# Kernel tuning notes

Measured on AMD Instinct MI355X. Metric: run time of the kernel, lower is better.

## Reference

```python
import jax, jax.numpy as jnp
import numpy as np

N = 50000        # nodes
E = 600000       # edges (before self loops)
F_IN = 128       # num_features
HID = 64         # hidden_channels
NC = 10          # num_classes
NG = 64          # graphs in batch
NEG_SLOPE = 0.2  # PyG GATv2 default


def setup_inputs() -> dict:
    key = jax.random.key(0)
    ks = jax.random.split(key, 13)
    s = lambda d: np.float32(1.0 / np.sqrt(d))
    x = jax.random.normal(ks[0], (N, F_IN), jnp.float32)
    edge_index = jax.random.randint(ks[1], (2, E), 0, N, dtype=jnp.int64)
    batch = jnp.sort(jax.random.randint(ks[2], (N,), 0, NG, dtype=jnp.int64))
    # conv1: heads=2, concat=True -> out dim 2*HID
    Wl1 = jax.random.normal(ks[3], (F_IN, 2 * HID), jnp.float32) * s(F_IN)
    Wr1 = jax.random.normal(ks[4], (F_IN, 2 * HID), jnp.float32) * s(F_IN)
    att1 = jax.random.normal(ks[5], (2, HID), jnp.float32) * s(HID)
    b1 = jnp.zeros((2 * HID,), jnp.float32)
    # conv2: heads=1, concat=False -> out dim HID
    Wl2 = jax.random.normal(ks[6], (2 * HID, HID), jnp.float32) * s(2 * HID)
    Wr2 = jax.random.normal(ks[7], (2 * HID, HID), jnp.float32) * s(2 * HID)
    att2 = jax.random.normal(ks[8], (1, HID), jnp.float32) * s(HID)
    b2 = jnp.zeros((HID,), jnp.float32)
    Wlin = jax.random.normal(ks[9], (HID, NC), jnp.float32) * s(HID)
    blin = jnp.zeros((NC,), jnp.float32)
    return {"x": x, "edge_index": edge_index, "batch": batch,
            "Wl1": Wl1, "Wr1": Wr1, "att1": att1, "b1": b1,
            "Wl2": Wl2, "Wr2": Wr2, "att2": att2, "b2": b2,
            "Wlin": Wlin, "blin": blin}


def _gatv2(x, Wl, Wr, att, b, src, dst, heads, ch, concat):
    """PyG GATv2Conv: e = a^T LeakyReLU(W_l x_j + W_r x_i), softmax over dst."""
    n = x.shape[0]
    xl = (x @ Wl).reshape(n, heads, ch)   # source-side transform
    xr = (x @ Wr).reshape(n, heads, ch)   # destination-side transform
    m = jax.nn.leaky_relu(xl[src] + xr[dst], NEG_SLOPE)  # [E, H, C]
    e = jnp.einsum('ehc,hc->eh', m, att)                 # [E, H]
    emax = jax.ops.segment_max(e, dst, num_segments=n)   # stable softmax per dst
    p = jnp.exp(e - emax[dst])
    denom = jax.ops.segment_sum(p, dst, num_segments=n)
    alpha = p / denom[dst]                               # [E, H]
    out = jax.ops.segment_sum(alpha[:, :, None] * xl[src], dst, num_segments=n)
    out = out.reshape(n, heads * ch) if concat else out.mean(axis=1)
    return out + b


def reference(x, edge_index, batch, Wl1, Wr1, att1, b1, Wl2, Wr2, att2, b2, Wlin, blin):
    loops = jnp.arange(N, dtype=edge_index.dtype)        # add_self_loops=True
    src = jnp.concatenate([edge_index[0], loops])
    dst = jnp.concatenate([edge_index[1], loops])
    h = jax.nn.elu(_gatv2(x, Wl1, Wr1, att1, b1, src, dst, 2, HID, True))
    h = jax.nn.elu(_gatv2(h, Wl2, Wr2, att2, b2, src, dst, 1, HID, False))
    # global_mean_pool
    pooled = jax.ops.segment_sum(h, batch, num_segments=NG)
    counts = jnp.maximum(
        jax.ops.segment_sum(jnp.ones((N,), h.dtype), batch, num_segments=NG), 1.0)
    g = pooled / counts[:, None]
    # dropout(p=0.4) is identity in eval mode
    return g @ Wlin + blin
```

## Files before the change

kernel.cpp:

```cpp
#include <hip/hip_runtime.h>
#include <hip/hip_fp16.h>
#include <cstdint>
#include <cstddef>


typedef __attribute__((ext_vector_type(8))) short s8v;
typedef __attribute__((ext_vector_type(4))) float f4v;

#define LOG2E 1.44269504f

__device__ __forceinline__ unsigned short f2bf(float f) {
    unsigned u = __float_as_uint(f);
    unsigned r = (u + 0x7fffu + ((u >> 16) & 1u)) >> 16;
    return (unsigned short)r;
}
__device__ __forceinline__ __half2 habs2_(__half2 x) {
    unsigned u; __builtin_memcpy(&u, &x, 4);
    u &= 0x7fff7fffu;
    __half2 r; __builtin_memcpy(&r, &u, 4);
    return r;
}
__device__ __forceinline__ float elu_(float v) {
    return v > 0.f ? v : exp2f(v * LOG2E) - 1.f;
}
union U4H { uint4 u; __half2 h[4]; };

template<int CO, bool ELU_A>
__device__ __forceinline__ void gemm_dual_body(
        int blk, const void* __restrict__ Aptr,
        const unsigned short* __restrict__ Wlp, const unsigned short* __restrict__ Wrp,
        __half* __restrict__ outL, __half* __restrict__ outR,
        const float* __restrict__ att, const float* __restrict__ bias_in,
        float* __restrict__ sl06, float* __restrict__ sr06, int n) {
    constexpr int NT = CO / 16;
    constexpr int H  = CO / 64;
    int lane = threadIdx.x & 63;
    int node0 = blk * 64 + (threadIdx.x >> 6) * 16;
    int m = lane & 15, quad = lane >> 4;
    int row = node0 + m;
    s8v a[4];
#pragma unroll
    for (int ks = 0; ks < 4; ks++) {
        union { s8v v; unsigned short u[8]; } t;
        int k0 = ks * 32 + quad * 8;
        if (row < n) {
            if (ELU_A) {
                const unsigned short* A = (const unsigned short*)Aptr;
                uint4 raw = *(const uint4*)(A + ((unsigned)row << 7) + k0);
                float4 bA = *(const float4*)(bias_in + k0);
                float4 bB = *(const float4*)(bias_in + k0 + 4);
                float bb[8] = {bA.x, bA.y, bA.z, bA.w, bB.x, bB.y, bB.z, bB.w};
                unsigned rr[4] = {raw.x, raw.y, raw.z, raw.w};
#pragma unroll
                for (int jp = 0; jp < 4; jp++) {
                    float e0 = elu_(__uint_as_float(rr[jp] << 16)         + bb[jp * 2]);
                    float e1 = elu_(__uint_as_float(rr[jp] & 0xffff0000u) + bb[jp * 2 + 1]);
                    t.u[jp * 2]     = f2bf(e0);
                    t.u[jp * 2 + 1] = f2bf(e1);
                }
            } else {
                const float* A = (const float*)Aptr;
                float4 fA = *(const float4*)(A + ((unsigned)row << 7) + k0);
                float4 fB = *(const float4*)(A + ((unsigned)row << 7) + k0 + 4);
                t.u[0] = f2bf(fA.x); t.u[1] = f2bf(fA.y);
                t.u[2] = f2bf(fA.z); t.u[3] = f2bf(fA.w);
                t.u[4] = f2bf(fB.x); t.u[5] = f2bf(fB.y);
                t.u[6] = f2bf(fB.z); t.u[7] = f2bf(fB.w);
            }
        } else {
#pragma unroll
            for (int j = 0; j < 8; j++) t.u[j] = 0;
        }
        a[ks] = t.v;
    }
    float dl[2] = {0.f, 0.f}, dr[2] = {0.f, 0.f};
#pragma unroll
    for (int ct = 0; ct < NT; ct++) {
        f4v cl = {0.f, 0.f, 0.f, 0.f}, cr = {0.f, 0.f, 0.f, 0.f};
#pragma unroll
        for (int ks = 0; ks < 4; ks++) {
            s8v bl = *(const s8v*)(Wlp + ((size_t)(ct * 4 + ks) * 64 + lane) * 8);
            s8v br = *(const s8v*)(Wrp + ((size_t)(ct * 4 + ks) * 64 + lane) * 8);
            cl = __builtin_amdgcn_mfma_f32_16x16x32_bf16(bl, a[ks], cl, 0, 0, 0);
            cr = __builtin_amdgcn_mfma_f32_16x16x32_bf16(br, a[ks], cr, 0, 0, 0);
        }
        int ch0 = ct * 16 + quad * 4;
        int hh = (H == 2) ? (ct >> 2) : 0;
        float4 av = *(const float4*)(att + ch0);
        dl[hh] += av.x * cl[0] + av.y * cl[1] + av.z * cl[2] + av.w * cl[3];
        dr[hh] += av.x * cr[0] + av.y * cr[1] + av.z * cr[2] + av.w * cr[3];
        if (row < n) {
            __half2 p0 = __floats2half2_rn(cl[0], cl[1]);
            __half2 p1 = __floats2half2_rn(cl[2], cl[3]);
            __half2 q0 = __floats2half2_rn(cr[0], cr[1]);
            __half2 q1 = __floats2half2_rn(cr[2], cr[3]);
            uint2 ov, orv;
            __builtin_memcpy(&ov.x, &p0, 4);  __builtin_memcpy(&ov.y, &p1, 4);
            __builtin_memcpy(&orv.x, &q0, 4); __builtin_memcpy(&orv.y, &q1, 4);
            *(uint2*)(outL + (unsigned)row * CO + ch0) = ov;
            *(uint2*)(outR + (unsigned)row * CO + ch0) = orv;
        }
    }
#pragma unroll
    for (int h = 0; h < H; h++) {
        float vl = dl[h], vr = dr[h];
        vl += __shfl_xor(vl, 16, 64); vl += __shfl_xor(vl, 32, 64);
        vr += __shfl_xor(vr, 16, 64); vr += __shfl_xor(vr, 32, 64);
        if (quad == 0 && row < n) {
            if (H == 2) {
                sl06[((unsigned)row << 1) + h] = (0.6f * LOG2E) * vl;
                sr06[((unsigned)row << 1) + h] = (0.6f * LOG2E) * vr;
            } else {
                sl06[row] = (0.6f * LOG2E) * vl;
                sr06[row] = (0.6f * LOG2E) * vr;
            }
        }
    }
}

__global__ void pack_zero(const float* __restrict__ Wl1, const float* __restrict__ Wr1,
                          const float* __restrict__ Wl2, const float* __restrict__ Wr2,
                          unsigned short* __restrict__ Wl1p, unsigned short* __restrict__ Wr1p,
                          unsigned short* __restrict__ Wl2p, unsigned short* __restrict__ Wr2p,
                          int* __restrict__ cnt, int n, int zcb,
                          float* __restrict__ pooled, int npool) {
    int b = blockIdx.x;
    if (b >= 24) {
        if (b < 24 + zcb) {
            int i = (b - 24) * 256 + threadIdx.x;
            if (i < n) cnt[i] = 0;
        } else {
            int i = (b - 24 - zcb) * 256 + threadIdx.x;
            if (i < npool) pooled[i] = 0.f;
        }
        return;
    }
    int t = b * 256 + threadIdx.x;
    const float* W; unsigned short* Wp; int CO, base;
    if      (t < 2048) { W = Wl1; Wp = Wl1p; CO = 128; base = t; }
    else if (t < 4096) { W = Wr1; Wp = Wr1p; CO = 128; base = t - 2048; }
    else if (t < 5120) { W = Wl2; Wp = Wl2p; CO = 64;  base = t - 4096; }
    else               { W = Wr2; Wp = Wr2p; CO = 64;  base = t - 5120; }
    int lane = base & 63, ks = (base >> 6) & 3, ct = base >> 8;
    int col = ct * 16 + (lane & 15);
    int k0 = ks * 32 + (lane >> 4) * 8;
    unsigned short u[8];
#pragma unroll
    for (int j = 0; j < 8; j++) u[j] = f2bf(W[(size_t)(k0 + j) * CO + col]);
    unsigned* dst = (unsigned*)(Wp + (size_t)base * 8);
    dst[0] = u[0] | ((unsigned)u[1] << 16);
    dst[1] = u[2] | ((unsigned)u[3] << 16);
    dst[2] = u[4] | ((unsigned)u[5] << 16);
    dst[3] = u[6] | ((unsigned)u[7] << 16);
}

__global__ void gemm1_fill(const float* __restrict__ x,
                           const unsigned short* __restrict__ Wl1p,
                           const unsigned short* __restrict__ Wr1p,
                           __half* __restrict__ xl1, __half* __restrict__ xr1,
                           const float* __restrict__ att1,
                           float* __restrict__ sl1, float* __restrict__ sr1, int n, int GB,
                           const int* __restrict__ srcA, const int* __restrict__ dstA, int E,
                           int* __restrict__ cnt, int* __restrict__ bucket) {
    if ((int)blockIdx.x < GB) {
        gemm_dual_body<128, false>(blockIdx.x, x, Wl1p, Wr1p, xl1, xr1,
                                   att1, nullptr, sl1, sr1, n);
        return;
    }
    int i = (blockIdx.x - GB) * 256 + threadIdx.x;
    if (i < E) {
        int d = dstA[i];
        int pos = atomicAdd(&cnt[d], 1);
        bucket[(d << 6) + pos] = srcA[i];
    }
}

__global__ void gemm2(const unsigned short* __restrict__ h1,
                      const unsigned short* __restrict__ Wl2p,
                      const unsigned short* __restrict__ Wr2p,
                      __half* __restrict__ xl2, __half* __restrict__ xr2,
                      const float* __restrict__ att2, const float* __restrict__ b1,
                      float* __restrict__ sl2, float* __restrict__ sr2, int n) {
    gemm_dual_body<64, true>(blockIdx.x, h1, Wl2p, Wr2p, xl2, xr2,
                             att2, b1, sl2, sr2, n);
}

__global__ void gat1_fused(const __half* __restrict__ xl, const __half* __restrict__ xr,
                           const float* __restrict__ sl06, const float* __restrict__ sr06,
                           const float* __restrict__ att,
                           const int* __restrict__ cnt, const int* __restrict__ bucket,
                           unsigned short* __restrict__ h1, int n) {
    int d = (blockIdx.x * blockDim.x + threadIdx.x) >> 6;
    if (d >= n) return;
    int lane = threadIdx.x & 63;
    int e = lane >> 4;
    int h = (lane >> 3) & 1;
    int off = h * 64 + (lane & 7) * 8;
    U4H xv; xv.u = *(const uint4*)(xr + (((unsigned)d << 7) + off));
    float4 aA = *(const float4*)(att + off);
    float4 aB = *(const float4*)(att + off + 4);
    const float S = 0.4f * LOG2E;
    __half2 a2[4];
    a2[0] = __floats2half2_rn(S * aA.x, S * aA.y);
    a2[1] = __floats2half2_rn(S * aA.z, S * aA.w);
    a2[2] = __floats2half2_rn(S * aB.x, S * aB.y);
    a2[3] = __floats2half2_rn(S * aB.z, S * aB.w);
    float srd = sr06[((unsigned)d << 1) + h];
    float c0 = 0.f, c1 = 0.f, c2 = 0.f, c3 = 0.f;
    float c4 = 0.f, c5 = 0.f, c6 = 0.f, c7 = 0.f, den = 0.f;
    int deg = cnt[d];
    int bb = d << 6;
    int j0 = -1 + e;
    int sA = bucket[bb + max(j0, 0)];  sA = (j0 >= 0 && j0 < deg) ? sA : d;
    int j1 = j0 + 4;
    int sB = bucket[bb + min(max(j1, 0), 63)];  sB = (j1 >= 0 && j1 < deg) ? sB : d;
    U4H xc; xc.u = *(const uint4*)(xl + (((unsigned)sA << 7) + off));
    float slc = sl06[((unsigned)sA << 1) + h];
    for (int base = -1; base < deg; base += 4) {
        U4H xn; xn.u = *(const uint4*)(xl + (((unsigned)sB << 7) + off));
        float sln = sl06[((unsigned)sB << 1) + h];
        int jC = base + 8 + e;
        int sC = bucket[bb + min(max(jC, 0), 63)];
        sC = (jC >= 0 && jC < deg) ? sC : d;
        bool valid = (base + e) < deg;
        __half2 sc = __floats2half2_rn(0.f, 0.f);
        sc = __hfma2(a2[0], habs2_(__hadd2(xc.h[0], xv.h[0])), sc);
        sc = __hfma2(a2[1], habs2_(__hadd2(xc.h[1], xv.h[1])), sc);
        sc = __hfma2(a2[2], habs2_(__hadd2(xc.h[2], xv.h[2])), sc);
        sc = __hfma2(a2[3], habs2_(__hadd2(xc.h[3], xv.h[3])), sc);
        float v = __low2float(sc) + __high2float(sc);
        v += __shfl_xor(v, 1, 64); v += __shfl_xor(v, 2, 64); v += __shfl_xor(v, 4, 64);
        float p = valid ? exp2f(slc + srd + v) : 0.f;
        c0 = fmaf(__low2float(xc.h[0]),  p, c0);
        c1 = fmaf(__high2float(xc.h[0]), p, c1);
        c2 = fmaf(__low2float(xc.h[1]),  p, c2);
        c3 = fmaf(__high2float(xc.h[1]), p, c3);
        c4 = fmaf(__low2float(xc.h[2]),  p, c4);
        c5 = fmaf(__high2float(xc.h[2]), p, c5);
        c6 = fmaf(__low2float(xc.h[3]),  p, c6);
        c7 = fmaf(__high2float(xc.h[3]), p, c7);
        den += p;
        xc = xn; slc = sln; sB = sC;
    }
#pragma unroll
    for (int o = 16; o <= 32; o <<= 1) {
        c0 += __shfl_xor(c0, o, 64); c1 += __shfl_xor(c1, o, 64);
        c2 += __shfl_xor(c2, o, 64); c3 += __shfl_xor(c3, o, 64);
        c4 += __shfl_xor(c4, o, 64); c5 += __shfl_xor(c5, o, 64);
        c6 += __shfl_xor(c6, o, 64); c7 += __shfl_xor(c7, o, 64);
        den += __shfl_xor(den, o, 64);
    }
    if (e == 0) {
        float r = 1.f / den;
        uint4 out;
        out.x = (unsigned)f2bf(c0 * r) | ((unsigned)f2bf(c1 * r) << 16);
        out.y = (unsigned)f2bf(c2 * r) | ((unsigned)f2bf(c3 * r) << 16);
        out.z = (unsigned)f2bf(c4 * r) | ((unsigned)f2bf(c5 * r) << 16);
        out.w = (unsigned)f2bf(c6 * r) | ((unsigned)f2bf(c7 * r) << 16);
        *(uint4*)(h1 + (((unsigned)d << 7) + off)) = out;
    }
}

__global__ void gat2_fused(const __half* __restrict__ xl, const __half* __restrict__ xr,
                           const float* __restrict__ sl06, const float* __restrict__ sr06,
                           const float* __restrict__ att,
                           const int* __restrict__ cnt, const int* __restrict__ bucket,
                           float* __restrict__ h2, int n) {
    int d = (blockIdx.x * blockDim.x + threadIdx.x) >> 6;
    if (d >= n) return;
    int lane = threadIdx.x & 63;
    int e = lane >> 3;
    int off = (lane & 7) * 8;
    U4H xv; xv.u = *(const uint4*)(xr + (((unsigned)d << 6) + off));
    float4 aA = *(const float4*)(att + off);
    float4 aB = *(const float4*)(att + off + 4);
    const float S = 0.4f * LOG2E;
    __half2 a2[4];
    a2[0] = __floats2half2_rn(S * aA.x, S * aA.y);
    a2[1] = __floats2half2_rn(S * aA.z, S * aA.w);
    a2[2] = __floats2half2_rn(S * aB.x, S * aB.y);
    a2[3] = __floats2half2_rn(S * aB.z, S * aB.w);
    float srd = sr06[d];
    float c0 = 0.f, c1 = 0.f, c2 = 0.f, c3 = 0.f;
    float c4 = 0.f, c5 = 0.f, c6 = 0.f, c7 = 0.f, den = 0.f;
    int deg = cnt[d];
    int bb = d << 6;
    int j0 = -1 + e;
    int sA = bucket[bb + max(j0, 0)];  sA = (j0 >= 0 && j0 < deg) ? sA : d;
    int j1 = j0 + 8;
    int sB = bucket[bb + min(max(j1, 0), 63)];  sB = (j1 >= 0 && j1 < deg) ? sB : d;
    U4H xc; xc.u = *(const uint4*)(xl + (((unsigned)sA << 6) + off));
    float slc = sl06[sA];
    for (int base = -1; base < deg; base += 8) {
        U4H xn; xn.u = *(const uint4*)(xl + (((unsigned)sB << 6) + off));
        float sln = sl06[sB];
        int jC = base + 16 + e;
        int sC = bucket[bb + min(max(jC, 0), 63)];
        sC = (jC >= 0 && jC < deg) ? sC : d;
        bool valid = (base + e) < deg;
        __half2 sc = __floats2half2_rn(0.f, 0.f);
        sc = __hfma2(a2[0], habs2_(__hadd2(xc.h[0], xv.h[0])), sc);
        sc = __hfma2(a2[1], habs2_(__hadd2(xc.h[1], xv.h[1])), sc);
        sc = __hfma2(a2[2], habs2_(__hadd2(xc.h[2], xv.h[2])), sc);
        sc = __hfma2(a2[3], habs2_(__hadd2(xc.h[3], xv.h[3])), sc);
        float v = __low2float(sc) + __high2float(sc);
        v += __shfl_xor(v, 1, 64); v += __shfl_xor(v, 2, 64); v += __shfl_xor(v, 4, 64);
        float p = valid ? exp2f(slc + srd + v) : 0.f;
        c0 = fmaf(__low2float(xc.h[0]),  p, c0);
        c1 = fmaf(__high2float(xc.h[0]), p, c1);
        c2 = fmaf(__low2float(xc.h[1]),  p, c2);
        c3 = fmaf(__high2float(xc.h[1]), p, c3);
        c4 = fmaf(__low2float(xc.h[2]),  p, c4);
        c5 = fmaf(__high2float(xc.h[2]), p, c5);
        c6 = fmaf(__low2float(xc.h[3]),  p, c6);
        c7 = fmaf(__high2float(xc.h[3]), p, c7);
        den += p;
        xc = xn; slc = sln; sB = sC;
    }
#pragma unroll
    for (int o = 8; o <= 32; o <<= 1) {
        c0 += __shfl_xor(c0, o, 64); c1 += __shfl_xor(c1, o, 64);
        c2 += __shfl_xor(c2, o, 64); c3 += __shfl_xor(c3, o, 64);
        c4 += __shfl_xor(c4, o, 64); c5 += __shfl_xor(c5, o, 64);
        c6 += __shfl_xor(c6, o, 64); c7 += __shfl_xor(c7, o, 64);
        den += __shfl_xor(den, o, 64);
    }
    if (e == 0) {
        float r = 1.f / den;
        float4 A = {c0 * r, c1 * r, c2 * r, c3 * r};
        float4 B = {c4 * r, c5 * r, c6 * r, c7 * r};
        *(float4*)(h2 + (((unsigned)d << 6) + off))     = A;
        *(float4*)(h2 + (((unsigned)d << 6) + off + 4)) = B;
    }
}

__global__ void pool_rle(const float* __restrict__ h, const float* __restrict__ b2,
                         const int* __restrict__ batch,
                         int n, int chunk, float* __restrict__ pooled,
                         float* __restrict__ counts) {
    int w = (blockIdx.x * blockDim.x + threadIdx.x) >> 6;
    int lane = threadIdx.x & 63;
    int start = w * chunk;
    int end = min(n, start + chunk);
    if (start >= end) return;
    float bv = b2[lane];
    int cur = batch[start];
    float acc = 0.f, cnt = 0.f;
    for (int node = start; node < end; node++) {
        int g = batch[node];
        if (g != cur) {
            atomicAdd(&pooled[(size_t)cur * 64 + lane], acc);
            if (lane == 0) atomicAdd(&counts[cur], cnt);
            acc = 0.f; cnt = 0.f; cur = g;
        }
        acc += elu_(h[((unsigned)node << 6) + lane] + bv);
        cnt += 1.f;
    }
    atomicAdd(&pooled[(size_t)cur * 64 + lane], acc);
    if (lane == 0) atomicAdd(&counts[cur], cnt);
}

__global__ void head(const float* __restrict__ pooled, const float* __restrict__ counts,
                     const float* __restrict__ Wlin, const float* __restrict__ blin,
                     float* __restrict__ out, int NC) {
    int g = blockIdx.x;
    int lane = threadIdx.x;
    float cnt = fmaxf(counts[g], 1.f);
    float v = pooled[(size_t)g * 64 + lane] / cnt;
    for (int j = 0; j < NC; j++) {
        float t = v * Wlin[lane * NC + j];
        for (int off = 32; off > 0; off >>= 1) t += __shfl_down(t, off, 64);
        if (lane == 0) out[g * NC + j] = t + blin[j];
    }
}

extern "C" void kernel_launch(void* const* d_in, const int* in_sizes, int n_in,
                              void* d_out, int out_size, void* d_ws, size_t ws_size,
                              hipStream_t stream) {
    const float* x    = (const float*)d_in[0];
    const int*   ei   = (const int*)d_in[1];
    const int*   batch= (const int*)d_in[2];
    const float* Wl1  = (const float*)d_in[3];
    const float* Wr1  = (const float*)d_in[4];
    const float* att1 = (const float*)d_in[5];
    const float* b1   = (const float*)d_in[6];
    const float* Wl2  = (const float*)d_in[7];
    const float* Wr2  = (const float*)d_in[8];
    const float* att2 = (const float*)d_in[9];
    const float* b2   = (const float*)d_in[10];
    const float* Wlin = (const float*)d_in[11];
    const float* blin = (const float*)d_in[12];

    const int n    = in_sizes[0] / 128;
    const int E    = in_sizes[1] / 2;
    const int NC   = in_sizes[12];
    const int NG   = out_size / NC;

    const int* srcA = ei;
    const int* dstA = ei + E;

    uint8_t* w = (uint8_t*)d_ws;
    const size_t rowB = (size_t)n * 128 * 2;
    __half*         xl1 = (__half*)w;
    __half*         xr1 = (__half*)(w + rowB);
    unsigned short* h1  = (unsigned short*)(w + 2 * rowB);
    __half*         xl2 = (__half*)w;
    __half*         xr2 = (__half*)(w + (size_t)n * 64 * 2);
    float*          h2  = (float*)(w + rowB);
    uint8_t* fx = w + 3 * rowB;
    unsigned short* Wl1p = (unsigned short*)fx;            fx += 16384 * 2;
    unsigned short* Wr1p = (unsigned short*)fx;            fx += 16384 * 2;
    unsigned short* Wl2p = (unsigned short*)fx;            fx += 8192 * 2;
    unsigned short* Wr2p = (unsigned short*)fx;            fx += 8192 * 2;
    float* sl1 = (float*)fx;                               fx += (size_t)n * 2 * 4;
    float* sr1 = (float*)fx;                               fx += (size_t)n * 2 * 4;
    float* sl2 = (float*)fx;                               fx += (size_t)n * 4;
    float* sr2 = (float*)fx;                               fx += (size_t)n * 4;
    float* pooled = (float*)fx;                            fx += (size_t)NG * 64 * 4;
    float* counts = (float*)fx;                            fx += (size_t)NG * 4;
    int* cnt    = (int*)fx;                                fx += (size_t)n * 4;
    int* bucket = (int*)fx;                                fx += ((size_t)n * 64 + 64) * 4;
    if (ws_size < (size_t)(fx - (uint8_t*)d_ws)) return;

    const int GB  = (n + 63) / 64;
    const int zcb = (n + 255) / 256;
    const int npool = NG * 65;
    const int pzb = (npool + 255) / 256;
    const int FB  = (E + 255) / 256;
    const int dblocks = (n + 3) / 4;

    pack_zero<<<24 + zcb + pzb, 256, 0, stream>>>(Wl1, Wr1, Wl2, Wr2,
                                                  Wl1p, Wr1p, Wl2p, Wr2p,
                                                  cnt, n, zcb, pooled, npool);
    gemm1_fill<<<GB + FB, 256, 0, stream>>>(x, Wl1p, Wr1p, xl1, xr1, att1,
                                            sl1, sr1, n, GB,
                                            srcA, dstA, E, cnt, bucket);
    gat1_fused<<<dblocks, 256, 0, stream>>>(xl1, xr1, sl1, sr1, att1,
                                            cnt, bucket, h1, n);
    gemm2<<<GB, 256, 0, stream>>>(h1, Wl2p, Wr2p, xl2, xr2, att2, b1, sl2, sr2, n);
    gat2_fused<<<dblocks, 256, 0, stream>>>(xl2, xr2, sl2, sr2, att2,
                                            cnt, bucket, h2, n);
    {
        const int nwaves = 1024;
        const int chunk = (n + nwaves - 1) / nwaves;
        pool_rle<<<256, 256, 0, stream>>>(h2, b2, batch, n, chunk, pooled, counts);
    }
    head<<<NG, 64, 0, stream>>>(pooled, counts, Wlin, blin, (float*)d_out, NC);
}
```

Before: 233.9 us.

## Interleave GEMM and edge-fill blocks, deepen gather prefetch, store h1 as fp16

The gemm1_fill launch now alternates GEMM blocks and edge-bucketing blocks by blockIdx parity, and each fill thread handles four edges, so the two kinds of work run side by side instead of GEMM blocks going first. Both GAT aggregation kernels now prefetch neighbour rows two iterations ahead instead of one, which should hide more gather latency at the cost of extra registers. The h1 intermediate is stored as fp16 instead of bf16, which makes packing cheaper and keeps more mantissa bits but has a smaller dynamic range.

```diff
diff --git a/kernel.cpp b/kernel.cpp
--- a/kernel.cpp
+++ b/kernel.cpp
@@ -45,16 +45,15 @@
         int k0 = ks * 32 + quad * 8;
         if (row < n) {
             if (ELU_A) {
-                const unsigned short* A = (const unsigned short*)Aptr;
-                uint4 raw = *(const uint4*)(A + ((unsigned)row << 7) + k0);
+                const __half* A = (const __half*)Aptr;
+                U4H raw; raw.u = *(const uint4*)(A + ((unsigned)row << 7) + k0);
                 float4 bA = *(const float4*)(bias_in + k0);
                 float4 bB = *(const float4*)(bias_in + k0 + 4);
                 float bb[8] = {bA.x, bA.y, bA.z, bA.w, bB.x, bB.y, bB.z, bB.w};
-                unsigned rr[4] = {raw.x, raw.y, raw.z, raw.w};
 #pragma unroll
                 for (int jp = 0; jp < 4; jp++) {
-                    float e0 = elu_(__uint_as_float(rr[jp] << 16)         + bb[jp * 2]);
-                    float e1 = elu_(__uint_as_float(rr[jp] & 0xffff0000u) + bb[jp * 2 + 1]);
+                    float e0 = elu_(__low2float(raw.h[jp])  + bb[jp * 2]);
+                    float e1 = elu_(__high2float(raw.h[jp]) + bb[jp * 2 + 1]);
                     t.u[jp * 2]     = f2bf(e0);
                     t.u[jp * 2 + 1] = f2bf(e1);
                 }
@@ -159,23 +158,34 @@
                            const unsigned short* __restrict__ Wr1p,
                            __half* __restrict__ xl1, __half* __restrict__ xr1,
                            const float* __restrict__ att1,
-                           float* __restrict__ sl1, float* __restrict__ sr1, int n, int GB,
+                           float* __restrict__ sl1, float* __restrict__ sr1, int n,
+                           int GB, int FBn,
                            const int* __restrict__ srcA, const int* __restrict__ dstA, int E,
                            int* __restrict__ cnt, int* __restrict__ bucket) {
-    if ((int)blockIdx.x < GB) {
-        gemm_dual_body<128, false>(blockIdx.x, x, Wl1p, Wr1p, xl1, xr1,
-                                   att1, nullptr, sl1, sr1, n);
+    int b = blockIdx.x;
+    if ((b & 1) == 0) {
+        int g = b >> 1;
+        if (g < GB)
+            gemm_dual_body<128, false>(g, x, Wl1p, Wr1p, xl1, xr1,
+                                       att1, nullptr, sl1, sr1, n);
         return;
     }
-    int i = (blockIdx.x - GB) * 256 + threadIdx.x;
-    if (i < E) {
-        int d = dstA[i];
-        int pos = atomicAdd(&cnt[d], 1);
-        bucket[(d << 6) + pos] = srcA[i];
-    }
-}
-
-__global__ void gemm2(const unsigned short* __restrict__ h1,
+    int f = b >> 1;
+    if (f >= FBn) return;
+    int t0 = f * 256 + threadIdx.x;
+    int Q = FBn * 256;
+#pragma unroll
+    for (int k = 0; k < 4; k++) {
+        int i = t0 + k * Q;
+        if (i < E) {
+            int d = dstA[i];
+            int pos = atomicAdd(&cnt[d], 1);
+            bucket[(d << 6) + pos] = srcA[i];
+        }
+    }
+}
+
+__global__ void gemm2(const __half* __restrict__ h1,
                       const unsigned short* __restrict__ Wl2p,
                       const unsigned short* __restrict__ Wr2p,
                       __half* __restrict__ xl2, __half* __restrict__ xr2,
@@ -189,7 +199,7 @@
                            const float* __restrict__ sl06, const float* __restrict__ sr06,
                            const float* __restrict__ att,
                            const int* __restrict__ cnt, const int* __restrict__ bucket,
-                           unsigned short* __restrict__ h1, int n) {
+                           __half* __restrict__ h1, int n) {
     int d = (blockIdx.x * blockDim.x + threadIdx.x) >> 6;
     if (d >= n) return;
     int lane = threadIdx.x & 63;
@@ -211,17 +221,21 @@
     int deg = cnt[d];
     int bb = d << 6;
     int j0 = -1 + e;
-    int sA = bucket[bb + max(j0, 0)];  sA = (j0 >= 0 && j0 < deg) ? sA : d;
+    int s0 = bucket[bb + max(j0, 0)];          s0 = (j0 >= 0 && j0 < deg) ? s0 : d;
     int j1 = j0 + 4;
-    int sB = bucket[bb + min(max(j1, 0), 63)];  sB = (j1 >= 0 && j1 < deg) ? sB : d;
-    U4H xc; xc.u = *(const uint4*)(xl + (((unsigned)sA << 7) + off));
-    float slc = sl06[((unsigned)sA << 1) + h];
+    int s1 = bucket[bb + min(max(j1, 0), 63)]; s1 = (j1 >= 0 && j1 < deg) ? s1 : d;
+    int j2 = j0 + 8;
+    int s2 = bucket[bb + min(max(j2, 0), 63)]; s2 = (j2 >= 0 && j2 < deg) ? s2 : d;
+    U4H xc;  xc.u  = *(const uint4*)(xl + (((unsigned)s0 << 7) + off));
+    float slc = sl06[((unsigned)s0 << 1) + h];
+    U4H xn1; xn1.u = *(const uint4*)(xl + (((unsigned)s1 << 7) + off));
+    float sln1 = sl06[((unsigned)s1 << 1) + h];
     for (int base = -1; base < deg; base += 4) {
-        U4H xn; xn.u = *(const uint4*)(xl + (((unsigned)sB << 7) + off));
-        float sln = sl06[((unsigned)sB << 1) + h];
-        int jC = base + 8 + e;
-        int sC = bucket[bb + min(max(jC, 0), 63)];
-        sC = (jC >= 0 && jC < deg) ? sC : d;
+        U4H xn2; xn2.u = *(const uint4*)(xl + (((unsigned)s2 << 7) + off));
+        float sln2 = sl06[((unsigned)s2 << 1) + h];
+        int j3 = base + 12 + e;
+        int s3 = bucket[bb + min(max(j3, 0), 63)];
+        s3 = (j3 >= 0 && j3 < deg) ? s3 : d;
         bool valid = (base + e) < deg;
         __half2 sc = __floats2half2_rn(0.f, 0.f);
         sc = __hfma2(a2[0], habs2_(__hadd2(xc.h[0], xv.h[0])), sc);
@@ -240,7 +254,7 @@
         c6 = fmaf(__low2float(xc.h[3]),  p, c6);
         c7 = fmaf(__high2float(xc.h[3]), p, c7);
         den += p;
-        xc = xn; slc = sln; sB = sC;
+        xc = xn1; slc = sln1; xn1 = xn2; sln1 = sln2; s2 = s3;
     }
 #pragma unroll
     for (int o = 16; o <= 32; o <<= 1) {
@@ -252,11 +266,13 @@
     }
     if (e == 0) {
         float r = 1.f / den;
+        __half2 o0 = __floats2half2_rn(c0 * r, c1 * r);
+        __half2 o1 = __floats2half2_rn(c2 * r, c3 * r);
+        __half2 o2 = __floats2half2_rn(c4 * r, c5 * r);
+        __half2 o3 = __floats2half2_rn(c6 * r, c7 * r);
         uint4 out;
-        out.x = (unsigned)f2bf(c0 * r) | ((unsigned)f2bf(c1 * r) << 16);
-        out.y = (unsigned)f2bf(c2 * r) | ((unsigned)f2bf(c3 * r) << 16);
-        out.z = (unsigned)f2bf(c4 * r) | ((unsigned)f2bf(c5 * r) << 16);
-        out.w = (unsigned)f2bf(c6 * r) | ((unsigned)f2bf(c7 * r) << 16);
+        __builtin_memcpy(&out.x, &o0, 4); __builtin_memcpy(&out.y, &o1, 4);
+        __builtin_memcpy(&out.z, &o2, 4); __builtin_memcpy(&out.w, &o3, 4);
         *(uint4*)(h1 + (((unsigned)d << 7) + off)) = out;
     }
 }
@@ -286,17 +302,21 @@
     int deg = cnt[d];
     int bb = d << 6;
     int j0 = -1 + e;
-    int sA = bucket[bb + max(j0, 0)];  sA = (j0 >= 0 && j0 < deg) ? sA : d;
+    int s0 = bucket[bb + max(j0, 0)];          s0 = (j0 >= 0 && j0 < deg) ? s0 : d;
     int j1 = j0 + 8;
-    int sB = bucket[bb + min(max(j1, 0), 63)];  sB = (j1 >= 0 && j1 < deg) ? sB : d;
-    U4H xc; xc.u = *(const uint4*)(xl + (((unsigned)sA << 6) + off));
-    float slc = sl06[sA];
+    int s1 = bucket[bb + min(max(j1, 0), 63)]; s1 = (j1 >= 0 && j1 < deg) ? s1 : d;
+    int j2 = j0 + 16;
+    int s2 = bucket[bb + min(max(j2, 0), 63)]; s2 = (j2 >= 0 && j2 < deg) ? s2 : d;
+    U4H xc;  xc.u  = *(const uint4*)(xl + (((unsigned)s0 << 6) + off));
+    float slc = sl06[s0];
+    U4H xn1; xn1.u = *(const uint4*)(xl + (((unsigned)s1 << 6) + off));
+    float sln1 = sl06[s1];
     for (int base = -1; base < deg; base += 8) {
-        U4H xn; xn.u = *(const uint4*)(xl + (((unsigned)sB << 6) + off));
-        float sln = sl06[sB];
-        int jC = base + 16 + e;
-        int sC = bucket[bb + min(max(jC, 0), 63)];
-        sC = (jC >= 0 && jC < deg) ? sC : d;
+        U4H xn2; xn2.u = *(const uint4*)(xl + (((unsigned)s2 << 6) + off));
+        float sln2 = sl06[s2];
+        int j3 = base + 24 + e;
+        int s3 = bucket[bb + min(max(j3, 0), 63)];
+        s3 = (j3 >= 0 && j3 < deg) ? s3 : d;
         bool valid = (base + e) < deg;
         __half2 sc = __floats2half2_rn(0.f, 0.f);
         sc = __hfma2(a2[0], habs2_(__hadd2(xc.h[0], xv.h[0])), sc);
@@ -315,7 +335,7 @@
         c6 = fmaf(__low2float(xc.h[3]),  p, c6);
         c7 = fmaf(__high2float(xc.h[3]), p, c7);
         den += p;
-        xc = xn; slc = sln; sB = sC;
+        xc = xn1; slc = sln1; xn1 = xn2; sln1 = sln2; s2 = s3;
     }
 #pragma unroll
     for (int o = 8; o <= 32; o <<= 1) {
@@ -403,7 +423,7 @@
     const size_t rowB = (size_t)n * 128 * 2;
     __half*         xl1 = (__half*)w;
     __half*         xr1 = (__half*)(w + rowB);
-    unsigned short* h1  = (unsigned short*)(w + 2 * rowB);
+    __half*         h1  = (__half*)(w + 2 * rowB);
     __half*         xl2 = (__half*)w;
     __half*         xr2 = (__half*)(w + (size_t)n * 64 * 2);
     float*          h2  = (float*)(w + rowB);
@@ -423,18 +443,19 @@
     if (ws_size < (size_t)(fx - (uint8_t*)d_ws)) return;
 
     const int GB  = (n + 63) / 64;
+    const int FBn = (E + 1023) / 1024;
     const int zcb = (n + 255) / 256;
     const int npool = NG * 65;
     const int pzb = (npool + 255) / 256;
-    const int FB  = (E + 255) / 256;
     const int dblocks = (n + 3) / 4;
+    const int T2 = 2 * max(GB, FBn);
 
     pack_zero<<<24 + zcb + pzb, 256, 0, stream>>>(Wl1, Wr1, Wl2, Wr2,
                                                   Wl1p, Wr1p, Wl2p, Wr2p,
                                                   cnt, n, zcb, pooled, npool);
-    gemm1_fill<<<GB + FB, 256, 0, stream>>>(x, Wl1p, Wr1p, xl1, xr1, att1,
-                                            sl1, sr1, n, GB,
-                                            srcA, dstA, E, cnt, bucket);
+    gemm1_fill<<<T2, 256, 0, stream>>>(x, Wl1p, Wr1p, xl1, xr1, att1,
+                                       sl1, sr1, n, GB, FBn,
+                                       srcA, dstA, E, cnt, bucket);
     gat1_fused<<<dblocks, 256, 0, stream>>>(xl1, xr1, sl1, sr1, att1,
                                             cnt, bucket, h1, n);
     gemm2<<<GB, 256, 0, stream>>>(h1, Wl2p, Wr2p, xl2, xr2, att2, b1, sl2, sr2, n);
```

New measurement: 236.2 us. Within noise of the previous version (+1.0%).
